# Kernel optimization log

Hardware: AMD Instinct MI355X
Metric: run time of the kernel (lower is better)

The kernel has to match this reference:

```python
import jax, jax.numpy as jnp
import numpy as np

B, C_HR, C_LR, HH, WH, HL, WL = 2, 256, 256, 128, 128, 64, 64
CC = 64            # compressed channels
LK, HK, EK = 5, 3, 3
GROUPS, LW, SCALE = 4, 3, 2


def conv2d(x, w, b, pad, dilation=1):
    out = jax.lax.conv_general_dilated(
        x, w, (1, 1), [(pad, pad), (pad, pad)],
        rhs_dilation=(dilation, dilation),
        dimension_numbers=('NCHW', 'OIHW', 'NCHW'))
    return out + b[None, :, None, None]


def unfold(x, k, dilation=1):
    # torch F.unfold with padding=(k//2)*dilation -> [B,C,k*k,H,W], row-major kernel order
    pad = (k // 2) * dilation
    Bb, C, H, W = x.shape
    xp = jnp.pad(x, ((0, 0), (0, 0), (pad, pad), (pad, pad)))
    patches = [xp[:, :, i * dilation:i * dilation + H, j * dilation:j * dilation + W]
               for i in range(k) for j in range(k)]
    return jnp.stack(patches, axis=2)


def kernel_normalizer(mask, k, hamming):
    n, c, h, w = mask.shape
    mc = c // (k * k)
    m = jax.nn.softmax(mask.reshape(n, mc, k * k, h, w), axis=2)
    m = m.reshape(n, mc, k, k, h, w) * hamming[None, None, :, :, None, None]
    m = m / jnp.sum(m, axis=(2, 3), keepdims=True)
    return m.reshape(n, c, h, w)


def carafe(feat, mask, k, scale):
    # mmcv CARAFE with group=1: mask at output resolution [B,k*k,H*s,W*s]
    Bb, C, H, W = feat.shape
    unf = unfold(feat, k)  # [B,C,k2,H,W]
    if scale == 1:
        return jnp.einsum('bckhw,bkhw->bchw', unf, mask)
    m = mask.reshape(Bb, k * k, H, scale, W, scale)
    out = jnp.einsum('bckhw,bkhpwq->bchpwq', unf, m)
    return out.reshape(Bb, C, H * scale, W * scale)


def group_norm(x, gamma, beta, groups, eps=1e-5):
    Bb, C, H, W = x.shape
    xg = x.reshape(Bb, groups, -1)
    mu = xg.mean(-1, keepdims=True)
    var = xg.var(-1, keepdims=True)
    xn = ((xg - mu) * jax.lax.rsqrt(var + eps)).reshape(Bb, C, H, W)
    return xn * gamma[None, :, None, None] + beta[None, :, None, None]


def compute_similarity(x, k=LW, dilation=2):
    unf = unfold(x, k, dilation)  # [B,C,k2,H,W]
    c = k * k // 2
    center = unf[:, :, c:c + 1]
    eps = 1e-8
    num = jnp.sum(center * unf, axis=1)
    den = (jnp.maximum(jnp.linalg.norm(center, axis=1), eps)
           * jnp.maximum(jnp.linalg.norm(unf, axis=1), eps))
    sim = num / den  # [B,k2,H,W]
    return jnp.concatenate([sim[:, :c], sim[:, c + 1:]], axis=1)


def pixel_shuffle(x, r):
    Bb, C, H, W = x.shape
    x = x.reshape(Bb, C // (r * r), r, r, H, W)
    return x.transpose(0, 1, 4, 2, 5, 3).reshape(Bb, C // (r * r), H * r, W * r)


def pixel_unshuffle(x, r):
    Bb, C, H, W = x.shape
    x = x.reshape(Bb, C, H // r, r, W // r, r)
    return x.transpose(0, 1, 3, 5, 2, 4).reshape(Bb, C * r * r, H // r, W // r)


def grid_sample_border(x, grid):
    # bilinear, padding_mode='border', align_corners=False; grid [N,Hg,Wg,2] (x,y)
    N, C, H, W = x.shape
    gx = jnp.clip((grid[..., 0] + 1.0) * W * 0.5 - 0.5, 0.0, W - 1.0)
    gy = jnp.clip((grid[..., 1] + 1.0) * H * 0.5 - 0.5, 0.0, H - 1.0)
    x0 = jnp.floor(gx); y0 = jnp.floor(gy)
    tx = (gx - x0)[:, None]; ty = (gy - y0)[:, None]
    x0i = x0.astype(jnp.int32); y0i = y0.astype(jnp.int32)
    x1i = jnp.minimum(x0i + 1, W - 1); y1i = jnp.minimum(y0i + 1, H - 1)
    g = jax.vmap(lambda img, yi, xi: img[:, yi, xi])
    v00 = g(x, y0i, x0i); v01 = g(x, y0i, x1i)
    v10 = g(x, y1i, x0i); v11 = g(x, y1i, x1i)
    return (v00 * (1 - tx) * (1 - ty) + v01 * tx * (1 - ty)
            + v10 * (1 - tx) * ty + v11 * tx * ty)


def init_pos():
    h = jnp.arange((-SCALE + 1) / 2, (SCALE - 1) / 2 + 1) / SCALE  # [-0.25, 0.25]
    t = jnp.stack(jnp.meshgrid(h, h, indexing='ij'))
    t = jnp.transpose(t, (0, 2, 1))
    return jnp.tile(t, (1, GROUPS, 1)).reshape(1, -1, 1, 1).astype(jnp.float32)


def dysampler(hr_x, lr_x, feat, gn_hr_w, gn_hr_b, gn_lr_w, gn_lr_b,
              w_off, b_off, w_hoff, b_hoff, w_ds, b_ds, w_hds, b_hds):
    hr_x = group_norm(hr_x, gn_hr_w, gn_hr_b, CC // 8)
    lr_x = group_norm(lr_x, gn_lr_w, gn_lr_b, CC // 8)
    hr_sim = compute_similarity(hr_x)
    lr_sim = compute_similarity(lr_x)
    pad = EK // 2
    off = conv2d(lr_sim, w_off, b_off, pad) + pixel_unshuffle(conv2d(hr_sim, w_hoff, b_hoff, pad), SCALE)
    ds = conv2d(lr_x, w_ds, b_ds, pad) + pixel_unshuffle(conv2d(hr_x, w_hds, b_hds, pad), SCALE)
    offset = off * jax.nn.sigmoid(ds) + init_pos()  # [B, 2*G*s^2, Hl, Wl]
    Bb, _, H, W = offset.shape
    off5 = offset.reshape(Bb, 2, -1, H, W)
    cw = jnp.arange(W, dtype=offset.dtype) + 0.5
    ch = jnp.arange(H, dtype=offset.dtype) + 0.5
    base = jnp.stack([jnp.broadcast_to(cw[None, :], (H, W)),
                      jnp.broadcast_to(ch[:, None], (H, W))])  # [2,H,W] (x,y)
    norm = jnp.array([W, H], offset.dtype).reshape(1, 2, 1, 1, 1)
    coords = 2.0 * (base[None, :, None] + off5) / norm - 1.0  # [B,2,G*s^2,H,W]
    coords = pixel_shuffle(coords.reshape(Bb, -1, H, W), SCALE)  # [B,2*G,sH,sW]
    coords = (coords.reshape(Bb, 2, GROUPS, SCALE * H, SCALE * W)
              .transpose(0, 2, 3, 4, 1)
              .reshape(Bb * GROUPS, SCALE * H, SCALE * W, 2))
    xs = feat.reshape(Bb * GROUPS, -1, feat.shape[-2], feat.shape[-1])
    out = grid_sample_border(xs, coords)
    return out.reshape(Bb, -1, SCALE * H, SCALE * W)


def setup_inputs() -> dict:
    key = jax.random.key(0)
    ks = jax.random.split(key, 16)
    r = lambda i, shape, s=0.05: jax.random.normal(ks[i], shape, jnp.float32) * s
    LC2, HC2 = LK * LK, HK * HK
    SIMC = LW * LW - 1
    OC = 2 * GROUPS * SCALE * SCALE
    OCH = 2 * GROUPS
    return {
        'hr_feat': jax.random.normal(ks[0], (B, C_HR, HH, WH), jnp.float32),
        'lr_feat': jax.random.normal(ks[1], (B, C_LR, HL, WL), jnp.float32),
        'w_hr_comp': r(2, (CC, C_HR, 1, 1)), 'b_hr_comp': r(3, (CC,)),
        'w_lr_comp': r(4, (CC, C_LR, 1, 1)), 'b_lr_comp': r(5, (CC,)),
        'w_enc': r(6, (LC2, CC, EK, EK), 0.01), 'b_enc': r(7, (LC2,), 0.01),
        'w_enc2': r(8, (HC2, CC, EK, EK), 0.01), 'b_enc2': r(9, (HC2,), 0.01),
        'gn_hr_w': jnp.ones((CC,), jnp.float32), 'gn_hr_b': jnp.zeros((CC,), jnp.float32),
        'gn_lr_w': jnp.ones((CC,), jnp.float32), 'gn_lr_b': jnp.zeros((CC,), jnp.float32),
        'w_off': r(10, (OC, SIMC, EK, EK), 0.01), 'b_off': jnp.zeros((OC,), jnp.float32),
        'w_hoff': r(11, (OCH, SIMC, EK, EK), 0.01), 'b_hoff': jnp.zeros((OCH,), jnp.float32),
        'w_ds': r(12, (OC, CC, EK, EK), 0.01), 'b_ds': jnp.zeros((OC,), jnp.float32),
        'w_hds': r(13, (OCH, CC, EK, EK), 0.01), 'b_hds': jnp.zeros((OCH,), jnp.float32),
    }


def reference(hr_feat, lr_feat, w_hr_comp, b_hr_comp, w_lr_comp, b_lr_comp,
              w_enc, b_enc, w_enc2, b_enc2, gn_hr_w, gn_hr_b, gn_lr_w, gn_lr_b,
              w_off, b_off, w_hoff, b_hoff, w_ds, b_ds, w_hds, b_hds):
    ham_lo = jnp.asarray(np.outer(np.hamming(LK), np.hamming(LK)), jnp.float32)
    ham_hi = jnp.asarray(np.outer(np.hamming(HK), np.hamming(HK)), jnp.float32)
    epad = EK // 2
    ch = conv2d(hr_feat, w_hr_comp, b_hr_comp, 0)
    cl = conv2d(lr_feat, w_lr_comp, b_lr_comp, 0)
    # semi_conv + comp_feat_upsample + use_high_pass path
    mask_hr_hr = conv2d(ch, w_enc2, b_enc2, epad)
    mh_init = kernel_normalizer(mask_hr_hr, HK, ham_hi)
    ch = 2.0 * ch - carafe(ch, mh_init, HK, 1)
    mask_lr_hr = conv2d(ch, w_enc, b_enc, epad)
    ml_init = kernel_normalizer(mask_lr_hr, LK, ham_lo)
    mask_lr_lr = carafe(conv2d(cl, w_enc, b_enc, epad), ml_init, LK, 2)
    mask_lr = mask_lr_hr + mask_lr_lr
    ml_init2 = kernel_normalizer(mask_lr, LK, ham_lo)
    mask_hr_lr = carafe(conv2d(cl, w_enc2, b_enc2, epad), ml_init2, LK, 2)
    mask_hr = mask_hr_hr + mask_hr_lr
    mask_lr_n = kernel_normalizer(mask_lr, LK, ham_lo)
    lr_up = carafe(lr_feat, mask_lr_n, LK, 2)
    mask_hr_n = kernel_normalizer(mask_hr, HK, ham_hi)
    hr_out = 2.0 * hr_feat - carafe(hr_feat, mask_hr_n, HK, 1)  # hr_residual
    lr_out = dysampler(ch, cl, lr_up, gn_hr_w, gn_hr_b, gn_lr_w, gn_lr_b,
                       w_off, b_off, w_hoff, b_hoff, w_ds, b_ds, w_hds, b_hds)
    return mask_lr_n, hr_out, lr_out
```

## Files before the change

kernel.cpp:

```cpp
#include <hip/hip_runtime.h>
#include <hip/hip_bf16.h>

typedef __hip_bfloat16 bf16;
#define TPB 256

__device__ __forceinline__ float toF(float v){ return v; }
__device__ __forceinline__ float toF(bf16 v){ return __bfloat162float(v); }
__device__ __forceinline__ float bfu(unsigned short u){
    unsigned int x = ((unsigned int)u) << 16;
    return __uint_as_float(x);
}
template<typename T> __device__ __forceinline__ void stT(T* p, long i, float v);
template<> __device__ __forceinline__ void stT<float>(float* p, long i, float v){ p[i] = v; }
template<> __device__ __forceinline__ void stT<bf16>(bf16* p, long i, float v){ p[i] = __float2bfloat16(v); }

static inline int nblk(long n){ return (int)((n + TPB - 1) / TPB); }

__global__ void k_detect(const void* hr, int n, int* flag, float* stat)
{
    if (threadIdx.x < 64) stat[threadIdx.x] = 0.f;
    const unsigned short* u = (const unsigned short*)hr;
    int nan = 0, oz = 0, ot = 0;
    for (int i = threadIdx.x; i < n; i += TPB) {
        unsigned short a = u[i] & 0x7FFF;
        if (a >= 0x7F80) nan++;
        if (i & 1) { ot++; if (a == 0) oz++; }
    }
    __shared__ int s1[TPB], s2[TPB], s3[TPB];
    s1[threadIdx.x] = nan; s2[threadIdx.x] = oz; s3[threadIdx.x] = ot;
    __syncthreads();
    if (threadIdx.x == 0) {
        int a = 0, b = 0, c = 0;
        for (int i = 0; i < TPB; i++) { a += s1[i]; b += s2[i]; c += s3[i]; }
        *flag = (a >= 6 || (long)b * 10 >= (long)c * 9) ? 1 : 0;
    }
}

#define P_W_HRC 0
#define P_B_HRC 16384
#define P_W_LRC 16448
#define P_B_LRC 32832
#define P_W_ENC 32896
#define P_B_ENC 47296
#define P_W_ENC2 47321
#define P_B_ENC2 52505
#define P_GNHW 52514
#define P_GNHB 52578
#define P_GNLW 52642
#define P_GNLB 52706
#define P_W_OFF 52770
#define P_B_OFF 55074
#define P_W_HOFF 55106
#define P_B_HOFF 55682
#define P_W_DS 55690
#define P_B_DS 74122
#define P_W_HDS 74154
#define P_B_HDS 78762
#define P_TOT 78770

__constant__ int c_segsz[20]  = {16384,64,16384,64,14400,25,5184,9,64,64,64,64,2304,32,576,8,18432,32,4608,8};
__constant__ int c_segbase[20]= {P_W_HRC,P_B_HRC,P_W_LRC,P_B_LRC,P_W_ENC,P_B_ENC,P_W_ENC2,P_B_ENC2,
                                 P_GNHW,P_GNHB,P_GNLW,P_GNLB,P_W_OFF,P_B_OFF,P_W_HOFF,P_B_HOFF,
                                 P_W_DS,P_B_DS,P_W_HDS,P_B_HDS};
__constant__ int c_segcin[20] = {256,0,256,0, 64,0, 64,0, 0,0,0,0, 8,0, 8,0, 64,0, 64,0};
__constant__ int c_segcout[20]= { 64,0, 64,0, 25,0,  9,0, 0,0,0,0,32,0, 8,0, 32,0,  8,0};
__constant__ int c_segtap[20] = {  1,0,  1,0,  9,0,  9,0, 0,0,0,0, 9,0, 9,0,  9,0,  9,0};

__global__ void k_prep(const void* p0,const void* p1,const void* p2,const void* p3,
                       const void* p4,const void* p5,const void* p6,const void* p7,
                       const void* p8,const void* p9,const void* p10,const void* p11,
                       const void* p12,const void* p13,const void* p14,const void* p15,
                       const void* p16,const void* p17,const void* p18,const void* p19,
                       float* dst, const int* flag)
{
    int idx = blockIdx.x * TPB + threadIdx.x;
    if (idx >= P_TOT) return;
    int s = 0, off = idx;
    while (off >= c_segsz[s]) { off -= c_segsz[s]; s++; }
    const void* sp;
    switch (s) {
        case 0: sp=p0; break;  case 1: sp=p1; break;  case 2: sp=p2; break;  case 3: sp=p3; break;
        case 4: sp=p4; break;  case 5: sp=p5; break;  case 6: sp=p6; break;  case 7: sp=p7; break;
        case 8: sp=p8; break;  case 9: sp=p9; break;  case 10: sp=p10; break; case 11: sp=p11; break;
        case 12: sp=p12; break; case 13: sp=p13; break; case 14: sp=p14; break; case 15: sp=p15; break;
        case 16: sp=p16; break; case 17: sp=p17; break; case 18: sp=p18; break; default: sp=p19; break;
    }
    float v = (*flag) ? ((const float*)sp)[off] : toF(((const bf16*)sp)[off]);
    int doff = off;
    int cin = c_segcin[s];
    if (cin) {
        int t = c_segtap[s], cout = c_segcout[s];
        int co = off / (cin * t);
        int r  = off % (cin * t);
        int ci = r / t, k = r % t;
        doff = (ci * cout + co) * t + k;
    }
    dst[c_segbase[s] + doff] = v;
}

template<typename T>
__device__ void transpLR_body(const T* __restrict__ x, bf16* __restrict__ xT, int Bn)
{
    __shared__ float tile[64][65];
    int bid = blockIdx.x;
    int pg = bid & 63;
    int cg = (bid >> 6) & 3;
    int b  = bid >> 8;
    int tid = threadIdx.x;
    int tr = tid >> 6, tc = tid & 63;
    for (int i = 0; i < 16; i++) {
        int c = tr + i * 4;
        tile[c][tc] = toF(x[(((long)(b * 256 + cg * 64 + c)) << 12) + (pg << 6) + tc]);
    }
    __syncthreads();
    for (int i = 0; i < 16; i++) {
        int p = tr + i * 4;
        xT[((((long)b << 12) + (pg << 6) + p) << 8) + (cg << 6) + tc] = __float2bfloat16(tile[tc][p]);
    }
}
__global__ void k_transpLR(const void* x, bf16* xT, int Bn, const int* flag)
{
    if (*flag) transpLR_body<float>((const float*)x, xT, Bn);
    else       transpLR_body<bf16 >((const bf16*)x,  xT, Bn);
}

__global__ void k_carafe5T(const bf16* __restrict__ featT, const float* __restrict__ mask,
                           bf16* __restrict__ outT, int Bn)
{
    int lane = threadIdx.x & 63;
    int wid = (blockIdx.x << 2) | (threadIdx.x >> 6);
    wid = __builtin_amdgcn_readfirstlane(wid);
    if (wid >= Bn * 4096 * 4) return;
    int q4   = wid & 3;
    int ipix = (wid >> 2) & 4095;
    int b    = wid >> 14;
    int h = ipix >> 6, w = ipix & 63;
    const bf16* fb = featT + (((long)b << 12) << 8);
    float f[25];
    #pragma unroll
    for (int i = 0; i < 5; i++) {
        int yy = h + i - 2; int yc = (yy >= 0 && yy < 64) ? yy : 0;
        #pragma unroll
        for (int j = 0; j < 5; j++) {
            int xx = w + j - 2; int xc = (xx >= 0 && xx < 64) ? xx : 0;
            f[i*5+j] = toF(fb[((long)((yc << 6) + xc) << 8) + (q4 << 6) + lane]);
        }
    }
    const float* mb = mask + (((long)b * 25) << 14);
    #pragma unroll
    for (int p = 0; p < 2; p++) {
        #pragma unroll
        for (int q = 0; q < 2; q++) {
            int opix = (((h << 1) + p) << 7) + (w << 1) + q;
            float acc = 0.f;
            #pragma unroll
            for (int k = 0; k < 25; k++) {
                int i = k / 5, j = k % 5;
                int yy = h + i - 2, xx = w + j - 2;
                bool v = (yy >= 0 && yy < 64 && xx >= 0 && xx < 64);
                float m = v ? mb[((long)k << 14) + opix] : 0.f;
                acc += f[k] * m;
            }
            outT[((((long)b << 14) + opix) << 8) + (q4 << 6) + lane] = __float2bfloat16(acc);
        }
    }
}

template<int COUT>
__global__ void k_conv3x3p(const float* __restrict__ x, const float* __restrict__ wf,
                           float* __restrict__ pbuf, int Bn, int CIN, int H, int W, int CS)
{
    int HW = H * W;
    int idx = blockIdx.x * TPB + threadIdx.x;
    if (idx >= Bn * HW) return;
    int chunk = blockIdx.y;
    int pix = idx % HW, b = idx / HW;
    int wx = pix % W, hy = pix / W;
    int off[9]; float msk[9];
    #pragma unroll
    for (int i = 0; i < 3; i++) {
        int yy = hy + i - 1; bool vy = (yy >= 0 && yy < H); int yc = vy ? yy : hy;
        #pragma unroll
        for (int j = 0; j < 3; j++) {
            int xx = wx + j - 1; bool v = vy && (xx >= 0 && xx < W);
            int xc = (xx >= 0 && xx < W) ? xx : wx;
            off[i*3+j] = yc * W + xc; msk[i*3+j] = v ? 1.f : 0.f;
        }
    }
    float acc[COUT];
    #pragma unroll
    for (int co = 0; co < COUT; co++) acc[co] = 0.f;
    int c0 = chunk * CS;
    const float* xb = x + ((long)b * CIN + c0) * HW;
    const float* wb = wf + (long)c0 * COUT * 9;
    #pragma unroll 2
    for (int ci = 0; ci < CS; ci++) {
        const float* xc = xb + (long)ci * HW;
        float t[9];
        #pragma unroll
        for (int k = 0; k < 9; k++) t[k] = xc[off[k]] * msk[k];
        const float* wr = wb + (long)ci * COUT * 9;
        #pragma unroll
        for (int co = 0; co < COUT; co++) {
            const float* wp = wr + co * 9;
            acc[co] += t[0]*wp[0] + t[1]*wp[1] + t[2]*wp[2] + t[3]*wp[3] + t[4]*wp[4]
                     + t[5]*wp[5] + t[6]*wp[6] + t[7]*wp[7] + t[8]*wp[8];
        }
    }
    long pb = ((long)chunk * Bn + b) * COUT * (long)HW + pix;
    #pragma unroll
    for (int co = 0; co < COUT; co++) pbuf[pb + (long)co * HW] = acc[co];
}

__global__ void k_convr(const float* __restrict__ pbuf, const float* __restrict__ bias,
                        float* __restrict__ out, int Bn, int COUT, int HW, int nChunk)
{
    long idx = (long)blockIdx.x * TPB + threadIdx.x;
    if (idx >= (long)Bn * COUT * HW) return;
    int pix = idx % HW;
    int co  = (idx / HW) % COUT;
    int b   = idx / ((long)HW * COUT);
    float v = bias[co];
    for (int ch = 0; ch < nChunk; ch++)
        v += pbuf[(((long)ch * Bn + b) * COUT + co) * HW + pix];
    out[idx] = v;
}

template<typename T>
__device__ void conv1x1p_body(const T* __restrict__ x, const float* __restrict__ wf,
                              float* __restrict__ pbuf, int Bn, int CIN, int HW, int CS)
{
    int idx = blockIdx.x * TPB + threadIdx.x;
    if (idx >= Bn * HW) return;
    int chunk = blockIdx.y;
    int pix = idx % HW, b = idx / HW;
    float acc[64];
    #pragma unroll
    for (int co = 0; co < 64; co++) acc[co] = 0.f;
    int c0 = chunk * CS;
    const T* xp = x + ((long)b * CIN + c0) * HW + pix;
    const float* wb = wf + (long)c0 * 64;
    #pragma unroll 2
    for (int ci = 0; ci < CS; ci++) {
        float v = toF(xp[(long)ci * HW]);
        const float* wr = wb + ci * 64;
        #pragma unroll
        for (int co = 0; co < 64; co++) acc[co] += v * wr[co];
    }
    long pb = ((long)chunk * Bn + b) * 64 * (long)HW + pix;
    #pragma unroll
    for (int co = 0; co < 64; co++) pbuf[pb + (long)co * HW] = acc[co];
}
__global__ void k_conv1x1p(const void* x, const float* wf, float* pbuf,
                           int Bn, int CIN, int HW, int CS, const int* flag)
{
    if (*flag) conv1x1p_body<float>((const float*)x, wf, pbuf, Bn, CIN, HW, CS);
    else       conv1x1p_body<bf16 >((const bf16*)x,  wf, pbuf, Bn, CIN, HW, CS);
}

template<int K, typename OT>
__device__ void knorm_body(const float* __restrict__ mask, float* __restrict__ out,
                           OT* __restrict__ outb, int B, int H, int W)
{
    const int K2 = K * K;
    int HWi = H * W;
    int idx = blockIdx.x * TPB + threadIdx.x;
    if (idx >= B * HWi) return;
    int pix = idx % HWi;
    int b   = idx / HWi;
    long HW = (long)HWi;
    long base = (long)b * K2 * HW + pix;
    float v[K2];
    float m = -1e30f;
    for (int k = 0; k < K2; k++) { v[k] = mask[base + k*HW]; m = fmaxf(m, v[k]); }
    float s2 = 0.f;
    for (int k = 0; k < K2; k++) {
        int i = k / K, j = k % K;
        float hi = (K == 3) ? ((i==1)?1.f:0.08f) : ((i==2)?1.f:((i==1||i==3)?0.54f:0.08f));
        float hj = (K == 3) ? ((j==1)?1.f:0.08f) : ((j==2)?1.f:((j==1||j==3)?0.54f:0.08f));
        v[k] = expf(v[k] - m) * hi * hj;
        s2 += v[k];
    }
    float inv = 1.f / s2;
    for (int k = 0; k < K2; k++) {
        float r = v[k] * inv;
        out[base + k*HW] = r;
        if (outb) stT<OT>(outb, base + k*HW, r);
    }
}
template<int K>
__global__ void k_knorm(const float* mask, float* out, void* outb, int B, int H, int W, const int* flag)
{
    if (*flag) knorm_body<K, float>(mask, out, (float*)outb, B, H, W);
    else       knorm_body<K, bf16>(mask, out, (bf16*)outb, B, H, W);
}

template<typename TF, typename TO, int NC>
__device__ void carafe3c_body(const TF* __restrict__ feat, const float* __restrict__ mask,
                              TO* __restrict__ out, int Bn)
{
    constexpr int CH = NC / 8;
    int idx = blockIdx.x * TPB + threadIdx.x;
    if (idx >= Bn * CH * 16384) return;
    int px = idx & 16383;
    int cc = (idx >> 14) % CH;
    int b  = (idx >> 14) / CH;
    int wx = px & 127, hy = px >> 7;
    float mk[9]; int off[9];
    #pragma unroll
    for (int i = 0; i < 3; i++) {
        int yy = hy + i - 1; bool vy = (yy >= 0 && yy < 128); int yc = vy ? yy : hy;
        #pragma unroll
        for (int j = 0; j < 3; j++) {
            int xx = wx + j - 1; bool v = vy && (xx >= 0 && xx < 128);
            int xc = (xx >= 0 && xx < 128) ? xx : wx;
            int k = i*3 + j;
            float m = mask[(((long)b*9 + k) << 14) + px];
            mk[k] = v ? m : 0.f;
            off[k] = (yc << 7) + xc;
        }
    }
    long base = ((long)(b * NC + cc * 8) << 14);
    for (int c = 0; c < 8; c++) {
        const TF* fp = feat + base + ((long)c << 14);
        float ctr = 0.f, acc = 0.f;
        #pragma unroll
        for (int k = 0; k < 9; k++) {
            float v = toF(fp[off[k]]);
            if (k == 4) ctr = v;
            acc += v * mk[k];
        }
        stT<TO>(out, base + ((long)c << 14) + px, 2.f * ctr - acc);
    }
}
__global__ void k_carafe3c_ws(const float* feat, const float* mask, float* out, int Bn)
{
    carafe3c_body<float, float, 64>(feat, mask, out, Bn);
}
__global__ void k_carafe3c_io(const void* feat, const float* mask, void* out, long outOff,
                              int Bn, const int* flag)
{
    if (*flag) carafe3c_body<float, float, 256>((const float*)feat, mask, (float*)out + outOff, Bn);
    else       carafe3c_body<bf16, bf16, 256>((const bf16*)feat, mask, (bf16*)out + outOff, Bn);
}

template<typename TF, typename TO, bool ADD, int CG>
__device__ void carafe5_body(const TF* __restrict__ feat, const float* __restrict__ mask,
                             const float* __restrict__ add, TO* __restrict__ out,
                             int Bn, int C)
{
    int ng = C / CG;
    int idx = blockIdx.x * TPB + threadIdx.x;
    if (idx >= Bn * ng * 16384) return;
    int px = idx & 16383;
    int gi = (idx >> 14) % ng;
    int b  = (idx >> 14) / ng;
    int X = px & 127, Y = px >> 7;
    int h = Y >> 1, w = X >> 1;
    float mk[25]; int off[25];
    const float* mb = mask + (((long)b * 25) << 14) + px;
    #pragma unroll
    for (int i = 0; i < 5; i++) {
        int yy = h + i - 2; bool vy = (yy >= 0 && yy < 64); int yc = vy ? yy : 0;
        #pragma unroll
        for (int j = 0; j < 5; j++) {
            int xx = w + j - 2; bool v = vy && (xx >= 0 && xx < 64);
            int xc = (xx >= 0 && xx < 64) ? xx : 0;
            int k = i*5 + j;
            mk[k] = v ? mb[(long)k << 14] : 0.f;
            off[k] = (yc << 6) + xc;
        }
    }
    int c0 = gi * CG;
    for (int c = 0; c < CG; c++) {
        long fb = ((long)(b * C + c0 + c) << 12);
        long ob = ((long)(b * C + c0 + c) << 14) + px;
        const TF* fp = feat + fb;
        float acc = ADD ? add[ob] : 0.f;
        #pragma unroll
        for (int k = 0; k < 25; k++) acc += toF(fp[off[k]]) * mk[k];
        stT<TO>(out, ob, acc);
    }
}
template<int CG>
__global__ void k_carafe5_ws(const float* feat, const float* mask, const float* add,
                             float* out, int Bn, int C)
{
    carafe5_body<float, float, true, CG>(feat, mask, add, out, Bn, C);
}

__global__ void k_gnstat(const float* __restrict__ x, float* __restrict__ stat, int statBase,
                         int S, int N)
{
    int bid = blockIdx.x;
    int bg = bid / S, sl = bid % S;
    int seg = N / S;
    long base = (long)bg * N + (long)sl * seg;
    float s = 0.f, ss = 0.f;
    for (int i = threadIdx.x; i < seg; i += TPB) {
        float v = x[base + i]; s += v; ss += v * v;
    }
    __shared__ float sh[8];
    for (int off = 32; off; off >>= 1) { s += __shfl_down(s, off); ss += __shfl_down(ss, off); }
    int wave = threadIdx.x >> 6, lane = threadIdx.x & 63;
    if (lane == 0) { sh[wave] = s; sh[4 + wave] = ss; }
    __syncthreads();
    if (threadIdx.x == 0) {
        float ts = 0.f, tss = 0.f;
        for (int i = 0; i < TPB/64; i++) { ts += sh[i]; tss += sh[4 + i]; }
        atomicAdd(&stat[statBase + bg*2], ts);
        atomicAdd(&stat[statBase + bg*2 + 1], tss);
    }
}
__global__ void k_gnapply(const float* __restrict__ x, const float* __restrict__ stat, int statBase,
                          const float* __restrict__ gamma, const float* __restrict__ beta,
                          float* __restrict__ out, int G, int Cg, int HW, int Bn)
{
    long idx = (long)blockIdx.x * TPB + threadIdx.x;
    long total = (long)Bn * G * Cg * HW;
    if (idx >= total) return;
    int bgN = Cg * HW;
    int bg = idx / bgN;
    int r  = idx % bgN;
    int g = bg % G;
    int c = g * Cg + r / HW;
    float s = stat[statBase + bg*2], ss = stat[statBase + bg*2 + 1];
    float mean = s / bgN;
    float inv = rsqrtf(ss / bgN - mean * mean + 1e-5f);
    out[idx] = (x[idx] - mean) * inv * gamma[c] + beta[c];
}

__global__ void k_simp(const float* __restrict__ x, float* __restrict__ pbuf,
                       int Bn, int H, int W, int CS)
{
    int HW = H * W;
    int idx = blockIdx.x * TPB + threadIdx.x;
    if (idx >= Bn * HW) return;
    int chunk = blockIdx.y;
    int pix = idx % HW, b = idx / HW;
    int wx = pix % W, hy = pix / W;
    const int dyv[8] = {-2,-2,-2, 0, 0, 2, 2, 2};
    const int dxv[8] = {-2, 0, 2,-2, 2,-2, 0, 2};
    int off[8]; float msk[8];
    #pragma unroll
    for (int n = 0; n < 8; n++) {
        int yy = hy + dyv[n], xx = wx + dxv[n];
        bool v = (yy >= 0 && yy < H && xx >= 0 && xx < W);
        off[n] = v ? yy * W + xx : pix;
        msk[n] = v ? 1.f : 0.f;
    }
    float dc = 0.f, num[8], dn[8];
    #pragma unroll
    for (int n = 0; n < 8; n++) { num[n] = 0.f; dn[n] = 0.f; }
    const float* xb = x + ((long)b * 64 + chunk * CS) * HW;
    #pragma unroll 2
    for (int ci = 0; ci < CS; ci++) {
        const float* xc = xb + (long)ci * HW;
        float c0 = xc[pix];
        dc += c0 * c0;
        #pragma unroll
        for (int n = 0; n < 8; n++) {
            float v = xc[off[n]] * msk[n];
            num[n] += c0 * v; dn[n] += v * v;
        }
    }
    long base = ((long)chunk * Bn + b) * 17 * (long)HW + pix;
    pbuf[base] = dc;
    #pragma unroll
    for (int n = 0; n < 8; n++) {
        pbuf[base + (long)(1 + n) * HW] = num[n];
        pbuf[base + (long)(9 + n) * HW] = dn[n];
    }
}
__global__ void k_simr(const float* __restrict__ pbuf, float* __restrict__ out,
                       int Bn, int HW, int nChunk)
{
    int idx = blockIdx.x * TPB + threadIdx.x;
    if (idx >= Bn * HW) return;
    int pix = idx % HW, b = idx / HW;
    float dc = 0.f, num[8], dn[8];
    #pragma unroll
    for (int n = 0; n < 8; n++) { num[n] = 0.f; dn[n] = 0.f; }
    for (int ch = 0; ch < nChunk; ch++) {
        long base = ((long)ch * Bn + b) * 17 * (long)HW + pix;
        dc += pbuf[base];
        #pragma unroll
        for (int n = 0; n < 8; n++) {
            num[n] += pbuf[base + (long)(1 + n) * HW];
            dn[n]  += pbuf[base + (long)(9 + n) * HW];
        }
    }
    float nc = fmaxf(sqrtf(dc), 1e-8f);
    #pragma unroll
    for (int n = 0; n < 8; n++)
        out[((long)(b*8 + n)) * HW + pix] = num[n] / (nc * fmaxf(sqrtf(dn[n]), 1e-8f));
}

__global__ void k_offset(const float* __restrict__ lro, const float* __restrict__ hro,
                         const float* __restrict__ lrd, const float* __restrict__ hrd,
                         float* __restrict__ outoff, int B)
{
    int idx = blockIdx.x * TPB + threadIdx.x;
    int total = B * 32 * 64 * 64;
    if (idx >= total) return;
    int wx = idx & 63;
    int hy = (idx >> 6) & 63;
    int o  = (idx >> 12) & 31;
    int b  = idx >> 17;
    int c = o >> 2, p = (o >> 1) & 1, q = o & 1;
    long hridx = ((long)(b*8 + c) * 128 + 2*hy + p) * 128 + 2*wx + q;
    float off = lro[idx] + hro[hridx];
    float dsv = lrd[idx] + hrd[hridx];
    float sg = 1.f / (1.f + expf(-dsv));
    int comp = o >> 4;
    float ip = (comp == 0) ? (q ? 0.25f : -0.25f) : (p ? 0.25f : -0.25f);
    outoff[idx] = off * sg + ip;
}

template<typename OT>
__device__ void gridsampleT_body(const unsigned short* __restrict__ lrupT,
                                 const float* __restrict__ offb, OT* __restrict__ out, int Bn)
{
    int idx = blockIdx.x * TPB + threadIdx.x;
    if (idx >= Bn * 4 * 16384) return;
    int ch0 = blockIdx.y << 5;
    int opix = idx & 16383;
    int g = (idx >> 14) & 3, b = idx >> 16;
    int X = opix & 127, Y = opix >> 7;
    int h = Y >> 1, p = Y & 1, w = X >> 1, q = X & 1;
    int r = g*4 + p*2 + q;
    float offx = offb[((long)(b*32 + r)      << 12) + (h << 6) + w];
    float offy = offb[((long)(b*32 + 16 + r) << 12) + (h << 6) + w];
    float gx = fminf(fmaxf(2.f * (w + 0.5f + offx) - 0.5f, 0.f), 127.f);
    float gy = fminf(fmaxf(2.f * (h + 0.5f + offy) - 0.5f, 0.f), 127.f);
    float x0f = floorf(gx), y0f = floorf(gy);
    float tx = gx - x0f, ty = gy - y0f;
    int x0 = (int)x0f, y0 = (int)y0f;
    int x1 = min(x0 + 1, 127), y1 = min(y0 + 1, 127);
    float w11 = tx * ty, w10 = ty - w11, w01 = tx - w11, w00 = 1.f - tx - ty + w11;
    const unsigned short* base = lrupT + (((long)b << 14) << 8) + (g << 6) + ch0;
    long a00 = ((long)((y0 << 7) + x0)) << 8, a01 = ((long)((y0 << 7) + x1)) << 8;
    long a10 = ((long)((y1 << 7) + x0)) << 8, a11 = ((long)((y1 << 7) + x1)) << 8;
    OT* op = out + ((long)(b * 256 + g * 64 + ch0) << 14) + opix;
    #pragma unroll
    for (int c8 = 0; c8 < 4; c8++) {
        uint4 v00 = *(const uint4*)(base + a00 + c8*8);
        uint4 v01 = *(const uint4*)(base + a01 + c8*8);
        uint4 v10 = *(const uint4*)(base + a10 + c8*8);
        uint4 v11 = *(const uint4*)(base + a11 + c8*8);
        const unsigned short* u00 = (const unsigned short*)&v00;
        const unsigned short* u01 = (const unsigned short*)&v01;
        const unsigned short* u10 = (const unsigned short*)&v10;
        const unsigned short* u11 = (const unsigned short*)&v11;
        #pragma unroll
        for (int t = 0; t < 8; t++) {
            float res = bfu(u00[t])*w00 + bfu(u01[t])*w01 + bfu(u10[t])*w10 + bfu(u11[t])*w11;
            stT<OT>(op, ((long)(c8*8 + t) << 14), res);
        }
    }
}
__global__ void k_gridsampleT(const bf16* lrupT, const float* offb, void* out, long outOff,
                              int Bn, const int* flag)
{
    if (*flag) gridsampleT_body<float>((const unsigned short*)lrupT, offb, (float*)out + outOff, Bn);
    else       gridsampleT_body<bf16 >((const unsigned short*)lrupT, offb, (bf16*)out + outOff, Bn);
}

extern "C" void kernel_launch(void* const* d_in, const int* in_sizes, int n_in,
                              void* d_out, int out_size, void* d_ws, size_t ws_size,
                              hipStream_t stream) {
    const void* hr_feat = d_in[0];
    const void* lr_feat = d_in[1];

    const int B = 2, HH = 128, HL = 64;
    const int HWH = HH*HH, HWL = HL*HL;

    int*   flag = (int*)d_ws;
    float* stat = (float*)d_ws + 4;
    float* P    = (float*)d_ws + 80;
    float* ws   = P + ((P_TOT + 63) & ~63);

    size_t o = 0;
    float* ch0    = ws + o; o += (size_t)B*64*HWH;
    float* clb    = ws + o; o += (size_t)B*64*HWL;
    float* maskHH = ws + o; o += (size_t)B*9*HWH;
    float* tmp9   = ws + o; o += (size_t)B*9*HWH;
    float* chn    = ws + o; o += (size_t)B*64*HWH;
    float* m25a   = ws + o; o += (size_t)B*25*HWH;
    float* m25b   = ws + o; o += (size_t)B*25*HWH;
    float* m25c   = ws + o; o += (size_t)B*25*HWH;
    float* enccl  = ws + o; o += (size_t)B*25*HWL;
    float* enc2cl = ws + o; o += (size_t)B*9*HWL;
    bf16*  lrupT  = (bf16*)(ws + o); o += (size_t)B*256*HWH/2;
    float* lrx    = ws + o; o += (size_t)B*64*HWL;
    float* hrsim  = ws + o; o += (size_t)B*8*HWH;
    float* lrsim  = ws + o; o += (size_t)B*8*HWL;
    float* qhro   = ws + o; o += (size_t)B*8*HWH;
    float* qlro   = ws + o; o += (size_t)B*32*HWL;
    float* qhrd   = ws + o; o += (size_t)B*8*HWH;
    float* qlrd   = ws + o; o += (size_t)B*32*HWL;
    float* offb   = ws + o; o += (size_t)B*32*HWL;
    float* hrx   = ch0;
    float* maskH = m25b;
    float* pbufA  = maskHH;
    float* pbuf3  = tmp9;
    float* pbuf6  = m25b;
    float* pbufL8 = (float*)lrupT;
    float* pbufT  = chn;
    bf16*  lrfT   = (bf16*)hrsim;
    (void)ws_size; (void)n_in;

    long out1Off = (long)B*25*HWH;
    long out2Off = out1Off + (long)B*256*HWH;

    const float* pw_hrc = P + P_W_HRC;  const float* pb_hrc = P + P_B_HRC;
    const float* pw_lrc = P + P_W_LRC;  const float* pb_lrc = P + P_B_LRC;
    const float* pw_enc = P + P_W_ENC;  const float* pb_enc = P + P_B_ENC;
    const float* pw_enc2= P + P_W_ENC2; const float* pb_enc2= P + P_B_ENC2;
    const float* pgnhw  = P + P_GNHW;   const float* pgnhb  = P + P_GNHB;
    const float* pgnlw  = P + P_GNLW;   const float* pgnlb  = P + P_GNLB;
    const float* pw_off = P + P_W_OFF;  const float* pb_off = P + P_B_OFF;
    const float* pw_hoff= P + P_W_HOFF; const float* pb_hoff= P + P_B_HOFF;
    const float* pw_ds  = P + P_W_DS;   const float* pb_ds  = P + P_B_DS;
    const float* pw_hds = P + P_W_HDS;  const float* pb_hds = P + P_B_HDS;

    int nDet = in_sizes[0] < 16384 ? in_sizes[0] : 16384;
    k_detect<<<1, TPB, 0, stream>>>(hr_feat, nDet, flag, stat);
    k_prep<<<nblk(P_TOT), TPB, 0, stream>>>(d_in[2],d_in[3],d_in[4],d_in[5],d_in[6],d_in[7],
        d_in[8],d_in[9],d_in[10],d_in[11],d_in[12],d_in[13],d_in[14],d_in[15],d_in[16],
        d_in[17],d_in[18],d_in[19],d_in[20],d_in[21], P, flag);
    k_transpLR<<<B*4*64, TPB, 0, stream>>>(lr_feat, lrfT, B, flag);

    k_conv1x1p<<<dim3(nblk((long)B*HWH),4), TPB, 0, stream>>>(hr_feat, pw_hrc, pbufA, B, 256, HWH, 64, flag);
    k_convr<<<nblk((long)B*64*HWH), TPB, 0, stream>>>(pbufA, pb_hrc, ch0, B, 64, HWH, 4);
    k_conv1x1p<<<dim3(nblk((long)B*HWL),16), TPB, 0, stream>>>(lr_feat, pw_lrc, pbufA, B, 256, HWL, 16, flag);
    k_convr<<<nblk((long)B*64*HWL), TPB, 0, stream>>>(pbufA, pb_lrc, clb, B, 64, HWL, 16);
    k_conv3x3p<9><<<dim3(nblk((long)B*HWH),8), TPB, 0, stream>>>(ch0, pw_enc2, pbuf3, B, 64, HH, HH, 8);
    k_convr<<<nblk((long)B*9*HWH), TPB, 0, stream>>>(pbuf3, pb_enc2, maskHH, B, 9, HWH, 8);
    k_knorm<3><<<nblk((long)B*HWH), TPB, 0, stream>>>(maskHH, tmp9, nullptr, B, HH, HH, flag);
    k_carafe3c_ws<<<nblk((long)B*8*16384), TPB, 0, stream>>>(ch0, tmp9, chn, B);
    k_conv3x3p<25><<<dim3(nblk((long)B*HWH),8), TPB, 0, stream>>>(chn, pw_enc, pbuf6, B, 64, HH, HH, 8);
    k_convr<<<nblk((long)B*25*HWH), TPB, 0, stream>>>(pbuf6, pb_enc, m25a, B, 25, HWH, 8);
    k_knorm<5><<<nblk((long)B*HWH), TPB, 0, stream>>>(m25a, m25b, nullptr, B, HH, HH, flag);
    k_conv3x3p<25><<<dim3(nblk((long)B*HWL),16), TPB, 0, stream>>>(clb, pw_enc, pbufL8, B, 64, HL, HL, 4);
    k_convr<<<nblk((long)B*25*HWL), TPB, 0, stream>>>(pbufL8, pb_enc, enccl, B, 25, HWL, 16);
    k_carafe5_ws<5><<<nblk((long)B*5*16384), TPB, 0, stream>>>(enccl, m25b, m25a, m25c, B, 25);
    k_knorm<5><<<nblk((long)B*HWH), TPB, 0, stream>>>(m25c, m25a, d_out, B, HH, HH, flag);
    k_conv3x3p<9><<<dim3(nblk((long)B*HWL),16), TPB, 0, stream>>>(clb, pw_enc2, pbufL8, B, 64, HL, HL, 4);
    k_convr<<<nblk((long)B*9*HWL), TPB, 0, stream>>>(pbufL8, pb_enc2, enc2cl, B, 9, HWL, 16);
    k_carafe5_ws<3><<<nblk((long)B*3*16384), TPB, 0, stream>>>(enc2cl, m25a, maskHH, maskH, B, 9);
    k_knorm<3><<<nblk((long)B*HWH), TPB, 0, stream>>>(maskH, tmp9, nullptr, B, HH, HH, flag);
    k_carafe3c_io<<<nblk((long)B*32*16384), TPB, 0, stream>>>(hr_feat, tmp9, d_out, out1Off, B, flag);
    k_carafe5T<<<B*4096*4/4, TPB, 0, stream>>>(lrfT, m25a, lrupT, B);
    k_gnstat<<<16*32, TPB, 0, stream>>>(chn, stat, 0, 32, 8*HWH);
    k_gnapply<<<nblk((long)B*64*HWH), TPB, 0, stream>>>(chn, stat, 0, pgnhw, pgnhb, hrx, 8, 8, HWH, B);
    k_gnstat<<<16*8, TPB, 0, stream>>>(clb, stat, 32, 8, 8*HWL);
    k_gnapply<<<nblk((long)B*64*HWL), TPB, 0, stream>>>(clb, stat, 32, pgnlw, pgnlb, lrx, 8, 8, HWL, B);
    k_simp<<<dim3(nblk((long)B*HWH),8), TPB, 0, stream>>>(hrx, pbufT, B, HH, HH, 8);
    k_simr<<<nblk((long)B*HWH), TPB, 0, stream>>>(pbufT, hrsim, B, HWH, 8);
    k_simp<<<dim3(nblk((long)B*HWL),16), TPB, 0, stream>>>(lrx, pbufT, B, HL, HL, 4);
    k_simr<<<nblk((long)B*HWL), TPB, 0, stream>>>(pbufT, lrsim, B, HWL, 16);
    k_conv3x3p<8><<<dim3(nblk((long)B*HWH),4), TPB, 0, stream>>>(hrsim, pw_hoff, pbufT, B, 8, HH, HH, 2);
    k_convr<<<nblk((long)B*8*HWH), TPB, 0, stream>>>(pbufT, pb_hoff, qhro, B, 8, HWH, 4);
    k_conv3x3p<32><<<dim3(nblk((long)B*HWL),8), TPB, 0, stream>>>(lrsim, pw_off, pbufT, B, 8, HL, HL, 1);
    k_convr<<<nblk((long)B*32*HWL), TPB, 0, stream>>>(pbufT, pb_off, qlro, B, 32, HWL, 8);
    k_conv3x3p<8><<<dim3(nblk((long)B*HWH),8), TPB, 0, stream>>>(hrx, pw_hds, pbufT, B, 64, HH, HH, 8);
    k_convr<<<nblk((long)B*8*HWH), TPB, 0, stream>>>(pbufT, pb_hds, qhrd, B, 8, HWH, 8);
    k_conv3x3p<32><<<dim3(nblk((long)B*HWL),16), TPB, 0, stream>>>(lrx, pw_ds, pbufT, B, 64, HL, HL, 4);
    k_convr<<<nblk((long)B*32*HWL), TPB, 0, stream>>>(pbufT, pb_ds, qlrd, B, 32, HWL, 16);
    k_offset<<<nblk((long)B*32*HWL), TPB, 0, stream>>>(qlro, qhro, qlrd, qhrd, offb, B);
    k_gridsampleT<<<dim3(nblk((long)B*4*HWH),2), TPB, 0, stream>>>(lrupT, offb, d_out, out2Off, B, flag);
}
```

Baseline: 667.0 us.

## Restructure CARAFE5 upsample: one wave per pixel, 4 channels per lane, vector loads

k_carafe5T now assigns one wavefront per input pixel, and each lane handles 4 consecutive channels instead of 1. The feature loads become 8-byte ushort4 reads, the mask loads become float2 reads, and each output is written as four packed bf16 values. The change cuts the number of mask loads per channel by 4x and widens memory transactions, at the cost of more registers per lane. It also adds an XCD-style swizzle of the block index and reduces the grid by 4x to match.

```diff
diff --git a/kernel.cpp b/kernel.cpp
--- a/kernel.cpp
+++ b/kernel.cpp
@@ -13,6 +13,19 @@
 template<typename T> __device__ __forceinline__ void stT(T* p, long i, float v);
 template<> __device__ __forceinline__ void stT<float>(float* p, long i, float v){ p[i] = v; }
 template<> __device__ __forceinline__ void stT<bf16>(bf16* p, long i, float v){ p[i] = __float2bfloat16(v); }
+
+__device__ __forceinline__ void st4bf(bf16* p, const float* a){
+    bf16 t0 = __float2bfloat16(a[0]);
+    bf16 t1 = __float2bfloat16(a[1]);
+    bf16 t2 = __float2bfloat16(a[2]);
+    bf16 t3 = __float2bfloat16(a[3]);
+    ushort4 pk;
+    pk.x = *(unsigned short*)&t0;
+    pk.y = *(unsigned short*)&t1;
+    pk.z = *(unsigned short*)&t2;
+    pk.w = *(unsigned short*)&t3;
+    *(ushort4*)p = pk;
+}
 
 static inline int nblk(long n){ return (int)((n + TPB - 1) / TPB); }
 
@@ -128,42 +141,42 @@
                            bf16* __restrict__ outT, int Bn)
 {
     int lane = threadIdx.x & 63;
-    int wid = (blockIdx.x << 2) | (threadIdx.x >> 6);
+    int nwg = gridDim.x;
+    int bid = blockIdx.x;
+    int swz = (nwg & 7) ? bid : ((bid & 7) * (nwg >> 3) + (bid >> 3));
+    int wid = (swz << 2) | (threadIdx.x >> 6);
     wid = __builtin_amdgcn_readfirstlane(wid);
-    if (wid >= Bn * 4096 * 4) return;
-    int q4   = wid & 3;
-    int ipix = (wid >> 2) & 4095;
-    int b    = wid >> 14;
+    if (wid >= Bn * 4096) return;
+    int ipix = wid & 4095;
+    int b    = wid >> 12;
     int h = ipix >> 6, w = ipix & 63;
-    const bf16* fb = featT + (((long)b << 12) << 8);
-    float f[25];
-    #pragma unroll
-    for (int i = 0; i < 5; i++) {
-        int yy = h + i - 2; int yc = (yy >= 0 && yy < 64) ? yy : 0;
-        #pragma unroll
-        for (int j = 0; j < 5; j++) {
-            int xx = w + j - 2; int xc = (xx >= 0 && xx < 64) ? xx : 0;
-            f[i*5+j] = toF(fb[((long)((yc << 6) + xc) << 8) + (q4 << 6) + lane]);
-        }
-    }
-    const float* mb = mask + (((long)b * 25) << 14);
-    #pragma unroll
-    for (int p = 0; p < 2; p++) {
-        #pragma unroll
-        for (int q = 0; q < 2; q++) {
-            int opix = (((h << 1) + p) << 7) + (w << 1) + q;
-            float acc = 0.f;
-            #pragma unroll
-            for (int k = 0; k < 25; k++) {
-                int i = k / 5, j = k % 5;
-                int yy = h + i - 2, xx = w + j - 2;
-                bool v = (yy >= 0 && yy < 64 && xx >= 0 && xx < 64);
-                float m = v ? mb[((long)k << 14) + opix] : 0.f;
-                acc += f[k] * m;
-            }
-            outT[((((long)b << 14) + opix) << 8) + (q4 << 6) + lane] = __float2bfloat16(acc);
-        }
-    }
+    const bf16*  fb = featT + (((long)b << 12) << 8) + (lane << 2);
+    const float* mb = mask + (((long)b * 25) << 14) + (h << 8) + (w << 1);
+    float a00[4], a01[4], a10[4], a11[4];
+    #pragma unroll
+    for (int t = 0; t < 4; t++) { a00[t]=0.f; a01[t]=0.f; a10[t]=0.f; a11[t]=0.f; }
+    #pragma unroll
+    for (int k = 0; k < 25; k++) {
+        const int i = k / 5, j = k % 5;
+        int yy = h + i - 2, xx = w + j - 2;
+        bool v = (yy >= 0 && yy < 64 && xx >= 0 && xx < 64);
+        int yc = v ? yy : 0, xc = v ? xx : 0;
+        ushort4 u = *(const ushort4*)(fb + ((long)((yc << 6) + xc) << 8));
+        float2 mr0 = *(const float2*)(mb + ((long)k << 14));
+        float2 mr1 = *(const float2*)(mb + ((long)k << 14) + 128);
+        float m00 = v ? mr0.x : 0.f, m01 = v ? mr0.y : 0.f;
+        float m10 = v ? mr1.x : 0.f, m11 = v ? mr1.y : 0.f;
+        float f0 = bfu(u.x), f1 = bfu(u.y), f2 = bfu(u.z), f3 = bfu(u.w);
+        a00[0] += f0*m00; a00[1] += f1*m00; a00[2] += f2*m00; a00[3] += f3*m00;
+        a01[0] += f0*m01; a01[1] += f1*m01; a01[2] += f2*m01; a01[3] += f3*m01;
+        a10[0] += f0*m10; a10[1] += f1*m10; a10[2] += f2*m10; a10[3] += f3*m10;
+        a11[0] += f0*m11; a11[1] += f1*m11; a11[2] += f2*m11; a11[3] += f3*m11;
+    }
+    bf16* op = outT + (((long)(b << 14) + (h << 8) + (w << 1)) << 8) + (lane << 2);
+    st4bf(op, a00);
+    st4bf(op + 256, a01);
+    st4bf(op + (128 << 8), a10);
+    st4bf(op + (128 << 8) + 256, a11);
 }
 
 template<int COUT>
@@ -651,7 +664,7 @@
     k_carafe5_ws<3><<<nblk((long)B*3*16384), TPB, 0, stream>>>(enc2cl, m25a, maskHH, maskH, B, 9);
     k_knorm<3><<<nblk((long)B*HWH), TPB, 0, stream>>>(maskH, tmp9, nullptr, B, HH, HH, flag);
     k_carafe3c_io<<<nblk((long)B*32*16384), TPB, 0, stream>>>(hr_feat, tmp9, d_out, out1Off, B, flag);
-    k_carafe5T<<<B*4096*4/4, TPB, 0, stream>>>(lrfT, m25a, lrupT, B);
+    k_carafe5T<<<B*4096/4, TPB, 0, stream>>>(lrfT, m25a, lrupT, B);
     k_gnstat<<<16*32, TPB, 0, stream>>>(chn, stat, 0, 32, 8*HWH);
     k_gnapply<<<nblk((long)B*64*HWH), TPB, 0, stream>>>(chn, stat, 0, pgnhw, pgnhb, hrx, 8, 8, HWH, B);
     k_gnstat<<<16*8, TPB, 0, stream>>>(clb, stat, 32, 8, 8*HWL);
```

New measurement: 571.2 us (median of 2 runs). -14.4%, faster.
